# Kernel tuning notes

Hardware: AMD Instinct MI355X
Metric: run time of the kernel (lower is better)

Reference implementation:

```python
import jax, jax.numpy as jnp
import numpy as np

B, L, H, E = 16, 4096, 8, 64
IN_CH, OUT_CH, MODES = 512, 512, 64


def setup_inputs() -> dict:
    key = jax.random.key(0)
    kq, kk, kv, k1, k2 = jax.random.split(key, 5)
    scale = 1.0 / (IN_CH * OUT_CH)
    q = jax.random.normal(kq, (B, L, H, E), jnp.float32)
    k = jax.random.normal(kk, (B, L, H, E), jnp.float32)
    v = jax.random.normal(kv, (B, L, H, E), jnp.float32)
    mask = jnp.zeros((B, L), jnp.bool_)
    # learned params: (heads=8, in_ch//8, out_ch//8, modes), torch.rand init * scale
    w1 = scale * jax.random.uniform(k1, (8, IN_CH // 8, OUT_CH // 8, MODES), jnp.float32)
    w2 = scale * jax.random.uniform(k2, (8, IN_CH // 8, OUT_CH // 8, MODES), jnp.float32)
    return {"q": q, "k": k, "v": v, "mask": mask, "w1": w1, "w2": w2}


def reference(q, k, v, mask, w1, w2):
    # q: [B, L, H, E]; k, v, mask unused by the original forward.
    Bq, Lq, Hq, Eq = q.shape
    modes = w1.shape[-1]
    x = jnp.transpose(q, (0, 2, 3, 1))          # [B, H, E, L]
    x_ft = jnp.fft.rfft(x, axis=-1)             # [B, H, E, L//2+1] complex64
    # mode_select_method='else' => index = [0..modes-1], wi == i, so the
    # per-mode gather/einsum/scatter loop collapses to a slice + batched einsum.
    sel = x_ft[..., :modes]                     # [B, H, E_in, modes]
    wc = w1 + 1j * w2                           # [H, E_in, E_out, modes] complex
    out_modes = jnp.einsum('bhim,hiom->bhom', sel, wc)  # [B, H, E_out, modes]
    nfreq = Lq // 2 + 1
    out_ft = jnp.zeros((Bq, Hq, w1.shape[2], nfreq), jnp.complex64)
    out_ft = out_ft.at[..., :modes].set(out_modes)
    x_out = jnp.fft.irfft(out_ft, n=Lq, axis=-1)  # [B, H, E_out, L] float32
    return x_out
```

## Files before the change

kernel.cpp:

```cpp
#include <hip/hip_runtime.h>
#include <math.h>

#define NB 16
#define NL 4096
#define NH 8
#define NI 64
#define NO 64
#define NM 64
#define QUARTER 1024
#define STEP 1.5339807878856412e-3f

using bf16_t = __bf16;
using bf16x8 = __attribute__((ext_vector_type(8))) __bf16;
using f32x16 = __attribute__((ext_vector_type(16))) float;

#define LDW 136
#define TMC 128

__global__ __launch_bounds__(256) void k_tab(float* __restrict__ ctab,
                                             bf16_t* __restrict__ Thi,
                                             bf16_t* __restrict__ Tlo) {
  const int gid = blockIdx.x * 256 + threadIdx.x;
  const int l = gid >> 7, mc = gid & 127, m = mc >> 1;
  const int p = (m * l) & 4095;
  const float c = cosf((float)p * STEP);
  const float s = cosf((float)((p + 3072) & 4095) * STEP);
  const float val = (mc & 1) ? -s : c;
  const bf16_t hi = (bf16_t)val;
  Thi[gid] = hi;
  Tlo[gid] = (bf16_t)(val - (float)hi);
  if (gid < 4096) ctab[gid] = cosf((float)gid * STEP);
}

__global__ __launch_bounds__(256) void k_fwd(const float* __restrict__ q,
                                             float* __restrict__ partial,
                                             const float* __restrict__ ctab,
                                             int LCF, int CHUNK) {
  const int lc = blockIdx.x, h = blockIdx.y, b = blockIdx.z;
  const int t = threadIdx.x;
  __shared__ float ct[4096];
  __shared__ float4 prep[16][64];

  for (int idx = t; idx < 4096; idx += 256) ct[idx] = ctab[idx];

  const int ig = t & 15;
  const int m0 = (t >> 4) << 2;
  float ar[4][4], ai[4][4];
#pragma unroll
  for (int k = 0; k < 4; ++k)
#pragma unroll
    for (int j = 0; j < 4; ++j) { ar[k][j] = 0.f; ai[k][j] = 0.f; }

  const int lstart = lc * CHUNK;

  for (int tt = 0; tt < CHUNK; tt += 16) {
    __syncthreads();
    {
      const int iA = t & 63;
#pragma unroll
      for (int c = 0; c < 4; ++c) {
        const int lloc = (t >> 6) + (c << 2);
        const int labs = lstart + tt + lloc;
        const float* qp = q + (((size_t)b * NL + labs) * NH + h) * NI + iA;
        const float q0 = qp[0];
        const float q1 = qp[(size_t)QUARTER * NH * NI];
        const float q2 = qp[(size_t)2 * QUARTER * NH * NI];
        const float q3 = qp[(size_t)3 * QUARTER * NH * NI];
        const float E = q0 + q2, F = q1 + q3;
        prep[lloc][iA] = make_float4(E + F, E - F, q0 - q2, q1 - q3);
      }
    }
    __syncthreads();
#pragma unroll 2
    for (int ll = 0; ll < 16; ++ll) {
      const int la = lstart + tt + ll;
      const int p0 = (m0 * la) & 4095;
      const int p1 = (p0 + la) & 4095;
      const int p2 = (p1 + la) & 4095;
      const int p3 = (p2 + la) & 4095;
      const float c0 = ct[p0], s0 = ct[(p0 + 3072) & 4095];
      const float c1 = ct[p1], s1 = ct[(p1 + 3072) & 4095];
      const float c2 = ct[p2], s2 = ct[(p2 + 3072) & 4095];
      const float c3 = ct[p3], s3 = ct[(p3 + 3072) & 4095];
#pragma unroll
      for (int j = 0; j < 4; ++j) {
        const float4 f = prep[ll][ig + (j << 4)];
        ar[0][j] = fmaf(f.x, c0, ar[0][j]);
        ai[0][j] = fmaf(-f.x, s0, ai[0][j]);
        ar[1][j] = fmaf(f.z, c1, ar[1][j]);
        ar[1][j] = fmaf(-f.w, s1, ar[1][j]);
        ai[1][j] = fmaf(-f.z, s1, ai[1][j]);
        ai[1][j] = fmaf(-f.w, c1, ai[1][j]);
        ar[2][j] = fmaf(f.y, c2, ar[2][j]);
        ai[2][j] = fmaf(-f.y, s2, ai[2][j]);
        ar[3][j] = fmaf(f.z, c3, ar[3][j]);
        ar[3][j] = fmaf(f.w, s3, ar[3][j]);
        ai[3][j] = fmaf(f.w, c3, ai[3][j]);
        ai[3][j] = fmaf(-f.z, s3, ai[3][j]);
      }
    }
  }
  float2* dst = (float2*)partial + (((size_t)b * NH + h) * LCF + lc) * (NM * NI);
#pragma unroll
  for (int k = 0; k < 4; ++k)
#pragma unroll
    for (int j = 0; j < 4; ++j)
      dst[(m0 + k) * NI + (ig + (j << 4))] = make_float2(ar[k][j], ai[k][j]);
}

__global__ __launch_bounds__(256) void k_mix(const float* __restrict__ partial,
                                             const float* __restrict__ w1,
                                             const float* __restrict__ w2,
                                             float* __restrict__ out2, int LCF) {
  const int og = blockIdx.x, h = blockIdx.y, b = blockIdx.z;
  const int t = threadIdx.x;
  __shared__ float sel_s[2][64][65];

  const float* src = partial + ((size_t)b * NH + h) * LCF * (NM * NI * 2);
  for (int u = t; u < NM * NI * 2; u += 256) {
    float v = 0.f;
    for (int lcx = 0; lcx < LCF; ++lcx) v += src[(size_t)lcx * (NM * NI * 2) + u];
    sel_s[u & 1][(u >> 1) & 63][u >> 7] = v;
  }
  __syncthreads();

  const int o = og * 16 + (t >> 4);
  const int mt = t & 15;
  float ar[4] = {0.f, 0.f, 0.f, 0.f}, ai[4] = {0.f, 0.f, 0.f, 0.f};
  for (int i = 0; i < NI; ++i) {
    const float* w1p = w1 + (((size_t)h * NI + i) * NO + o) * NM;
    const float* w2p = w2 + (((size_t)h * NI + i) * NO + o) * NM;
#pragma unroll
    for (int k = 0; k < 4; ++k) {
      const int m = mt + (k << 4);
      const float re = sel_s[0][i][m];
      const float im = sel_s[1][i][m];
      const float a = w1p[m];
      const float bb = w2p[m];
      ar[k] = fmaf(re, a, ar[k]);
      ar[k] = fmaf(-im, bb, ar[k]);
      ai[k] = fmaf(re, bb, ai[k]);
      ai[k] = fmaf(im, a, ai[k]);
    }
  }
  float2* dst = (float2*)out2 + ((size_t)b * NH + h) * (NM * NO);
#pragma unroll
  for (int k = 0; k < 4; ++k)
    dst[(mt + (k << 4)) * NO + o] = make_float2(ar[k], ai[k]);
}

__global__ __launch_bounds__(256) void k_inv(const float* __restrict__ out2,
                                             const bf16_t* __restrict__ Thi,
                                             const bf16_t* __restrict__ Tlo,
                                             float* __restrict__ xout) {
  const int lb = blockIdx.x, h = blockIdx.y, b = blockIdx.z;
  const int t = threadIdx.x;
  __shared__ bf16_t Whi[64 * LDW];
  __shared__ bf16_t Wlo[64 * LDW];

  {
    const float2* src = (const float2*)out2 + ((size_t)b * NH + h) * (NM * NO);
    for (int u = t; u < NM * NO; u += 256) {
      const int m = u >> 6, o = u & 63;
      const float fac = (m == 0 ? 1.0f : 2.0f) * (1.0f / 4096.0f);
      const float2 cc = src[u];
      const float re = cc.x * fac, im = cc.y * fac;
      const bf16_t reh = (bf16_t)re, imh = (bf16_t)im;
      Whi[o * LDW + 2 * m] = reh;
      Whi[o * LDW + 2 * m + 1] = imh;
      Wlo[o * LDW + 2 * m] = (bf16_t)(re - (float)reh);
      Wlo[o * LDW + 2 * m + 1] = (bf16_t)(im - (float)imh);
    }
  }
  __syncthreads();

  const int w = t >> 6, lane = t & 63;
  const int lrow = lane & 31;
  const int kh = (lane >> 5) << 3;
  const int lwave = (lb << 8) + (w << 6);

  f32x16 acc[2][2] = {};

#pragma unroll
  for (int ks = 0; ks < 8; ++ks) {
    const int kb = ks * 16 + kh;
    const bf16x8 ah0 = *(const bf16x8*)&Whi[lrow * LDW + kb];
    const bf16x8 ah1 = *(const bf16x8*)&Whi[(lrow + 32) * LDW + kb];
    const bf16x8 al0 = *(const bf16x8*)&Wlo[lrow * LDW + kb];
    const bf16x8 al1 = *(const bf16x8*)&Wlo[(lrow + 32) * LDW + kb];
    const size_t r0 = (size_t)(lwave + lrow) * TMC + kb;
    const size_t r1 = (size_t)(lwave + 32 + lrow) * TMC + kb;
    const bf16x8 bh0 = *(const bf16x8*)&Thi[r0];
    const bf16x8 bh1 = *(const bf16x8*)&Thi[r1];
    const bf16x8 bl0 = *(const bf16x8*)&Tlo[r0];
    const bf16x8 bl1 = *(const bf16x8*)&Tlo[r1];
#define MM(a, bb, c) c = __builtin_amdgcn_mfma_f32_32x32x16_bf16(a, bb, c, 0, 0, 0)
    MM(ah0, bh0, acc[0][0]); MM(ah0, bl0, acc[0][0]); MM(al0, bh0, acc[0][0]);
    MM(ah0, bh1, acc[0][1]); MM(ah0, bl1, acc[0][1]); MM(al0, bh1, acc[0][1]);
    MM(ah1, bh0, acc[1][0]); MM(ah1, bl0, acc[1][0]); MM(al1, bh0, acc[1][0]);
    MM(ah1, bh1, acc[1][1]); MM(ah1, bl1, acc[1][1]); MM(al1, bh1, acc[1][1]);
#undef MM
  }

  float* obase = xout + ((size_t)b * NH + h) * NO * (size_t)NL;
#pragma unroll
  for (int of = 0; of < 2; ++of)
#pragma unroll
    for (int lf = 0; lf < 2; ++lf) {
      const int lg = lwave + lf * 32 + lrow;
#pragma unroll
      for (int r = 0; r < 16; ++r) {
        const int o = of * 32 + (r & 3) + 8 * (r >> 2) + 4 * (lane >> 5);
        obase[(size_t)o * NL + lg] = acc[of][lf][r];
      }
    }
}

extern "C" void kernel_launch(void* const* d_in, const int* in_sizes, int n_in,
                              void* d_out, int out_size, void* d_ws, size_t ws_size,
                              hipStream_t stream) {
  const float* q  = (const float*)d_in[0];
  const float* w1 = (const float*)d_in[4];
  const float* w2 = (const float*)d_in[5];
  float* out = (float*)d_out;

  const size_t out2Elems = (size_t)NB * NH * NM * NO * 2;
  const size_t tElems = (size_t)NL * TMC;
  const size_t tabFloats = 4096 + (2 * tElems * sizeof(bf16_t)) / sizeof(float);
  int LCF = 1;
  const int cands[4] = {8, 4, 2, 1};
  for (int ci = 0; ci < 4; ++ci) {
    const size_t pe = (size_t)NB * NH * cands[ci] * NM * NI * 2;
    if ((pe + out2Elems + tabFloats) * sizeof(float) <= ws_size) { LCF = cands[ci]; break; }
  }
  const size_t partialElems = (size_t)NB * NH * LCF * NM * NI * 2;
  float* partial = (float*)d_ws;
  float* out2 = partial + partialElems;
  float* ctab = out2 + out2Elems;
  bf16_t* Thi = (bf16_t*)(ctab + 4096);
  bf16_t* Tlo = Thi + tElems;

  dim3 blk(256);
  k_tab<<<dim3((unsigned)(tElems / 256)), blk, 0, stream>>>(ctab, Thi, Tlo);
  k_fwd<<<dim3(LCF, NH, NB), blk, 0, stream>>>(q, partial, ctab, LCF, QUARTER / LCF);
  k_mix<<<dim3(4, NH, NB), blk, 0, stream>>>(partial, w1, w2, out2, LCF);
  k_inv<<<dim3(16, NH, NB), blk, 0, stream>>>(out2, Thi, Tlo, out);
}
```

Measured before the change: 496.5 us.

## Compute forward truncated DFT with bf16x3 MFMA against precomputed twiddle table

Replaces the scalar FMA forward DFT, which used a radix-4 pre-split of q and an LDS cosine table, with a matrix multiply on MFMA 32x32x16 bf16 instructions. A new transposed twiddle table is built in split hi/lo bf16 form, and q is split into hi/lo bf16 on load. Three MFMAs per tile (hi*hi, hi*lo, lo*hi) approximate fp32 precision. This drops the radix-4 symmetry, so the K dimension becomes the full 4096 samples, and it adds twiddle table memory traffic in exchange for matrix-core throughput.

Result: no change. 486.9 us (-1.9%).

```diff
diff --git a/kernel.cpp b/kernel.cpp
--- a/kernel.cpp
+++ b/kernel.cpp
@@ -7,7 +7,6 @@
 #define NI 64
 #define NO 64
 #define NM 64
-#define QUARTER 1024
 #define STEP 1.5339807878856412e-3f
 
 using bf16_t = __bf16;
@@ -17,95 +16,103 @@
 #define LDW 136
 #define TMC 128
 
-__global__ __launch_bounds__(256) void k_tab(float* __restrict__ ctab,
-                                             bf16_t* __restrict__ Thi,
-                                             bf16_t* __restrict__ Tlo) {
+__global__ __launch_bounds__(256) void k_tab(bf16_t* __restrict__ Thi,
+                                             bf16_t* __restrict__ Tlo,
+                                             bf16_t* __restrict__ Tfhi,
+                                             bf16_t* __restrict__ Tflo) {
   const int gid = blockIdx.x * 256 + threadIdx.x;
-  const int l = gid >> 7, mc = gid & 127, m = mc >> 1;
-  const int p = (m * l) & 4095;
-  const float c = cosf((float)p * STEP);
-  const float s = cosf((float)((p + 3072) & 4095) * STEP);
-  const float val = (mc & 1) ? -s : c;
-  const bf16_t hi = (bf16_t)val;
-  Thi[gid] = hi;
-  Tlo[gid] = (bf16_t)(val - (float)hi);
-  if (gid < 4096) ctab[gid] = cosf((float)gid * STEP);
+  {
+    const int l = gid >> 7, mc = gid & 127, m = mc >> 1;
+    const int p = (m * l) & 4095;
+    const float c = cosf((float)p * STEP);
+    const float s = cosf((float)((p + 3072) & 4095) * STEP);
+    const float val = (mc & 1) ? -s : c;
+    const bf16_t hi = (bf16_t)val;
+    Thi[gid] = hi;
+    Tlo[gid] = (bf16_t)(val - (float)hi);
+  }
+  {
+    const int mc = gid >> 12, l = gid & 4095, m = mc >> 1;
+    const int p = (m * l) & 4095;
+    const float c = cosf((float)p * STEP);
+    const float s = cosf((float)((p + 3072) & 4095) * STEP);
+    const float val = (mc & 1) ? -s : c;
+    const bf16_t hi = (bf16_t)val;
+    Tfhi[gid] = hi;
+    Tflo[gid] = (bf16_t)(val - (float)hi);
+  }
 }
 
 __global__ __launch_bounds__(256) void k_fwd(const float* __restrict__ q,
                                              float* __restrict__ partial,
-                                             const float* __restrict__ ctab,
-                                             int LCF, int CHUNK) {
+                                             const bf16_t* __restrict__ Tfhi,
+                                             const bf16_t* __restrict__ Tflo,
+                                             int LCF, int KCH) {
   const int lc = blockIdx.x, h = blockIdx.y, b = blockIdx.z;
   const int t = threadIdx.x;
-  __shared__ float ct[4096];
-  __shared__ float4 prep[16][64];
-
-  for (int idx = t; idx < 4096; idx += 256) ct[idx] = ctab[idx];
-
-  const int ig = t & 15;
-  const int m0 = (t >> 4) << 2;
-  float ar[4][4], ai[4][4];
-#pragma unroll
-  for (int k = 0; k < 4; ++k)
-#pragma unroll
-    for (int j = 0; j < 4; ++j) { ar[k][j] = 0.f; ai[k][j] = 0.f; }
-
-  const int lstart = lc * CHUNK;
-
-  for (int tt = 0; tt < CHUNK; tt += 16) {
+  __shared__ uint32_t Bh[64][33], Bl[64][33];
+
+  const int w = t >> 6, lane = t & 63;
+  const int arow = lane & 31;
+  const int kh = (lane >> 5) << 3;
+  const int lp = t & 31;
+  const int i0 = (t >> 5) << 3;
+
+  f32x16 acc[2] = {};
+
+  const int lbase0 = lc * KCH;
+  const bf16_t* Ah = Tfhi + (size_t)(w * 32 + arow) * NL + lbase0 + kh;
+  const bf16_t* Al = Tflo + (size_t)(w * 32 + arow) * NL + lbase0 + kh;
+
+  for (int ks = 0; ks < KCH; ks += 64) {
     __syncthreads();
     {
-      const int iA = t & 63;
-#pragma unroll
-      for (int c = 0; c < 4; ++c) {
-        const int lloc = (t >> 6) + (c << 2);
-        const int labs = lstart + tt + lloc;
-        const float* qp = q + (((size_t)b * NL + labs) * NH + h) * NI + iA;
-        const float q0 = qp[0];
-        const float q1 = qp[(size_t)QUARTER * NH * NI];
-        const float q2 = qp[(size_t)2 * QUARTER * NH * NI];
-        const float q3 = qp[(size_t)3 * QUARTER * NH * NI];
-        const float E = q0 + q2, F = q1 + q3;
-        prep[lloc][iA] = make_float4(E + F, E - F, q0 - q2, q1 - q3);
+      const int l0 = lbase0 + ks + (lp << 1);
+      const float* qp = q + (((size_t)b * NL + l0) * NH + h) * NI + i0;
+      const float4 a0 = *(const float4*)qp;
+      const float4 a1 = *(const float4*)(qp + 4);
+      const float4 b0 = *(const float4*)(qp + NH * NI);
+      const float4 b1 = *(const float4*)(qp + NH * NI + 4);
+      const float va[8] = {a0.x, a0.y, a0.z, a0.w, a1.x, a1.y, a1.z, a1.w};
+      const float vb[8] = {b0.x, b0.y, b0.z, b0.w, b1.x, b1.y, b1.z, b1.w};
+#pragma unroll
+      for (int j = 0; j < 8; ++j) {
+        const bf16_t h0 = (bf16_t)va[j], h1 = (bf16_t)vb[j];
+        const bf16_t g0 = (bf16_t)(va[j] - (float)h0);
+        const bf16_t g1 = (bf16_t)(vb[j] - (float)h1);
+        union { bf16_t u[2]; uint32_t w32; } ph, pl;
+        ph.u[0] = h0; ph.u[1] = h1;
+        pl.u[0] = g0; pl.u[1] = g1;
+        Bh[i0 + j][lp] = ph.w32;
+        Bl[i0 + j][lp] = pl.w32;
       }
     }
     __syncthreads();
-#pragma unroll 2
-    for (int ll = 0; ll < 16; ++ll) {
-      const int la = lstart + tt + ll;
-      const int p0 = (m0 * la) & 4095;
-      const int p1 = (p0 + la) & 4095;
-      const int p2 = (p1 + la) & 4095;
-      const int p3 = (p2 + la) & 4095;
-      const float c0 = ct[p0], s0 = ct[(p0 + 3072) & 4095];
-      const float c1 = ct[p1], s1 = ct[(p1 + 3072) & 4095];
-      const float c2 = ct[p2], s2 = ct[(p2 + 3072) & 4095];
-      const float c3 = ct[p3], s3 = ct[(p3 + 3072) & 4095];
-#pragma unroll
-      for (int j = 0; j < 4; ++j) {
-        const float4 f = prep[ll][ig + (j << 4)];
-        ar[0][j] = fmaf(f.x, c0, ar[0][j]);
-        ai[0][j] = fmaf(-f.x, s0, ai[0][j]);
-        ar[1][j] = fmaf(f.z, c1, ar[1][j]);
-        ar[1][j] = fmaf(-f.w, s1, ar[1][j]);
-        ai[1][j] = fmaf(-f.z, s1, ai[1][j]);
-        ai[1][j] = fmaf(-f.w, c1, ai[1][j]);
-        ar[2][j] = fmaf(f.y, c2, ar[2][j]);
-        ai[2][j] = fmaf(-f.y, s2, ai[2][j]);
-        ar[3][j] = fmaf(f.z, c3, ar[3][j]);
-        ar[3][j] = fmaf(f.w, s3, ar[3][j]);
-        ai[3][j] = fmaf(f.w, c3, ai[3][j]);
-        ai[3][j] = fmaf(-f.z, s3, ai[3][j]);
-      }
-    }
-  }
-  float2* dst = (float2*)partial + (((size_t)b * NH + h) * LCF + lc) * (NM * NI);
-#pragma unroll
-  for (int k = 0; k < 4; ++k)
-#pragma unroll
-    for (int j = 0; j < 4; ++j)
-      dst[(m0 + k) * NI + (ig + (j << 4))] = make_float2(ar[k][j], ai[k][j]);
+#pragma unroll
+    for (int kk = 0; kk < 4; ++kk) {
+      const bf16x8 ah = *(const bf16x8*)(Ah + ks + kk * 16);
+      const bf16x8 al = *(const bf16x8*)(Al + ks + kk * 16);
+      const int wd = (kk * 16 + kh) >> 1;
+      const bf16x8 bh0 = *(const bf16x8*)&Bh[arow][wd];
+      const bf16x8 bl0 = *(const bf16x8*)&Bl[arow][wd];
+      const bf16x8 bh1 = *(const bf16x8*)&Bh[arow + 32][wd];
+      const bf16x8 bl1 = *(const bf16x8*)&Bl[arow + 32][wd];
+#define MM(a, bb, c) c = __builtin_amdgcn_mfma_f32_32x32x16_bf16(a, bb, c, 0, 0, 0)
+      MM(ah, bh0, acc[0]); MM(ah, bl0, acc[0]); MM(al, bh0, acc[0]);
+      MM(ah, bh1, acc[1]); MM(ah, bl1, acc[1]); MM(al, bh1, acc[1]);
+#undef MM
+    }
+  }
+
+  float* pdst = partial + (((size_t)b * NH + h) * LCF + lc) * (NM * NI * 2);
+#pragma unroll
+  for (int ihf = 0; ihf < 2; ++ihf)
+#pragma unroll
+    for (int r = 0; r < 16; ++r) {
+      const int mc = w * 32 + (r & 3) + 8 * (r >> 2) + 4 * (lane >> 5);
+      const int i = arow + ihf * 32;
+      pdst[(mc >> 1) * (NI * 2) + i * 2 + (mc & 1)] = acc[ihf][r];
+    }
 }
 
 __global__ __launch_bounds__(256) void k_mix(const float* __restrict__ partial,
@@ -225,8 +232,8 @@
   float* out = (float*)d_out;
 
   const size_t out2Elems = (size_t)NB * NH * NM * NO * 2;
-  const size_t tElems = (size_t)NL * TMC;
-  const size_t tabFloats = 4096 + (2 * tElems * sizeof(bf16_t)) / sizeof(float);
+  const size_t tE = 524288;
+  const size_t tabFloats = (4 * tE) / 2;
   int LCF = 1;
   const int cands[4] = {8, 4, 2, 1};
   for (int ci = 0; ci < 4; ++ci) {
@@ -236,13 +243,14 @@
   const size_t partialElems = (size_t)NB * NH * LCF * NM * NI * 2;
   float* partial = (float*)d_ws;
   float* out2 = partial + partialElems;
-  float* ctab = out2 + out2Elems;
-  bf16_t* Thi = (bf16_t*)(ctab + 4096);
-  bf16_t* Tlo = Thi + tElems;
+  bf16_t* Thi = (bf16_t*)(out2 + out2Elems);
+  bf16_t* Tlo = Thi + tE;
+  bf16_t* Tfhi = Tlo + tE;
+  bf16_t* Tflo = Tfhi + tE;
 
   dim3 blk(256);
-  k_tab<<<dim3((unsigned)(tElems / 256)), blk, 0, stream>>>(ctab, Thi, Tlo);
-  k_fwd<<<dim3(LCF, NH, NB), blk, 0, stream>>>(q, partial, ctab, LCF, QUARTER / LCF);
+  k_tab<<<dim3((unsigned)(tE / 256)), blk, 0, stream>>>(Thi, Tlo, Tfhi, Tflo);
+  k_fwd<<<dim3(LCF, NH, NB), blk, 0, stream>>>(q, partial, Tfhi, Tflo, LCF, NL / LCF);
   k_mix<<<dim3(4, NH, NB), blk, 0, stream>>>(partial, w1, w2, out2, LCF);
   k_inv<<<dim3(16, NH, NB), blk, 0, stream>>>(out2, Thi, Tlo, out);
 }
```
